# Performance work log

Measured on AMD Instinct MI355X. Metric: run time of the kernel, lower is better.

## Reference

```python
import jax, jax.numpy as jnp
import numpy as np

LAMBDA_0 = 1.0
EPS = 1e-6


def setup_inputs() -> dict:
    key = jax.random.key(0)
    ks = jax.random.split(key, 5)
    B, T, D, H = 4, 2048, 1024, 128
    x = jax.random.normal(ks[0], (B, T, D), dtype=jnp.float32)
    Wq = jax.random.normal(ks[1], (H, D), dtype=jnp.float32) * (D ** -0.5)
    Wk = jax.random.normal(ks[2], (H, D), dtype=jnp.float32) * (D ** -0.5)
    Wv = jax.random.normal(ks[3], (H, D), dtype=jnp.float32) * (D ** -0.5)
    Wo = jax.random.normal(ks[4], (D, H), dtype=jnp.float32) * (H ** -0.5)
    bq = jnp.zeros((H,), jnp.float32)
    bk = jnp.zeros((H,), jnp.float32)
    bv = jnp.zeros((H,), jnp.float32)
    bo = jnp.zeros((D,), jnp.float32)
    return {"x": x, "Wq": Wq, "bq": bq, "Wk": Wk, "bk": bk, "Wv": Wv, "bv": bv, "Wo": Wo, "bo": bo}


def reference(x, Wq, bq, Wk, bk, Wv, bv, Wo, bo):
    B, T, D = x.shape
    H = Wq.shape[0]
    # Projections for all timesteps at once (equivalent to per-step Linear calls)
    Q = jnp.einsum('btd,hd->bth', x, Wq) + bq
    K = jnp.einsum('btd,hd->bth', x, Wk) + bk
    V = jnp.einsum('btd,hd->bth', x, Wv) + bv

    A0 = jnp.broadcast_to(jnp.eye(H, dtype=jnp.float32) / LAMBDA_0, (B, H, H))  # (lambda_0 I)^-1
    M0 = jnp.zeros((B, H, H), jnp.float32)

    def step(carry, qkv):
        A, M = carry
        q, k, v = qkv                                  # each (B,H)
        s_t = jnp.sum(k * q, axis=-1, keepdims=True)   # (B,1)
        # PenaltyBuilder (rank-1): unit direction of k
        u = k / (jnp.linalg.norm(k, axis=-1, keepdims=True) + EPS)
        # Sherman-Morrison update: A <- A - (A u)(A u)^T / (1 + u^T A u)
        Au = jnp.einsum('bij,bj->bi', A, u)            # (B,H)
        denom = 1.0 + jnp.sum(u * Au, axis=-1, keepdims=True)  # (B,1)
        A = A - jnp.einsum('bi,bj->bij', Au, Au) / denom[..., None]
        # z = A_new @ u == Au / denom (exact identity, saves a matvec)
        z = Au / denom
        alpha = s_t * z                                # (B,H)
        M = M + jnp.einsum('bi,bj->bij', v, alpha)     # memory matrix accumulation
        o = jnp.einsum('bij,bj->bi', M, q)             # (B,H)
        return (A, M), o

    qkv = (jnp.swapaxes(Q, 0, 1), jnp.swapaxes(K, 0, 1), jnp.swapaxes(V, 0, 1))  # (T,B,H)
    _, O = jax.lax.scan(step, (A0, M0), qkv)
    O = jnp.swapaxes(O, 0, 1)                          # (B,T,H)
    return jnp.einsum('bth,dh->btd', O, Wo) + bo
```

## Files before the change

### kernel.cpp

```cpp
#include <hip/hip_runtime.h>
#include <math.h>

#define BB 4
#define TT 2048
#define DD 1024
#define HH 128
#define EPSF 1e-6f
#define BT (BB*TT)

__global__ __launch_bounds__(256) void proj_kernel(
    const float* __restrict__ x,
    const float* __restrict__ Wq, const float* __restrict__ bq,
    const float* __restrict__ Wk, const float* __restrict__ bk,
    const float* __restrict__ Wv, const float* __restrict__ bv,
    float* __restrict__ Q, float* __restrict__ K, float* __restrict__ V)
{
    const int which = blockIdx.y;
    const float* W    = (which == 0) ? Wq : (which == 1) ? Wk : Wv;
    const float* bias = (which == 0) ? bq : (which == 1) ? bk : bv;
    float* P          = (which == 0) ? Q  : (which == 1) ? K  : V;

    const int row0 = blockIdx.x * 64;

    __shared__ float xT[32][68];
    __shared__ float wT[32][132];

    const int tid = threadIdx.x;
    const int tx = tid & 15;
    const int ty = tid >> 4;

    float acc[4][8];
    #pragma unroll
    for (int i = 0; i < 4; i++)
        #pragma unroll
        for (int j = 0; j < 8; j++) acc[i][j] = 0.f;

    for (int k0 = 0; k0 < DD; k0 += 32) {
        #pragma unroll
        for (int l = 0; l < 2; l++) {
            int f = tid + l * 256;
            int r = f >> 3;
            int cg = f & 7;
            float4 v = *(const float4*)(x + (size_t)(row0 + r) * DD + k0 + cg * 4);
            xT[cg*4+0][r] = v.x; xT[cg*4+1][r] = v.y;
            xT[cg*4+2][r] = v.z; xT[cg*4+3][r] = v.w;
        }
        #pragma unroll
        for (int l = 0; l < 4; l++) {
            int f = tid + l * 256;
            int h = f >> 3;
            int cg = f & 7;
            float4 v = *(const float4*)(W + (size_t)h * DD + k0 + cg * 4);
            wT[cg*4+0][h] = v.x; wT[cg*4+1][h] = v.y;
            wT[cg*4+2][h] = v.z; wT[cg*4+3][h] = v.w;
        }
        __syncthreads();
        #pragma unroll
        for (int kk = 0; kk < 32; kk++) {
            float4 xv = *(const float4*)&xT[kk][ty * 4];
            float4 w0 = *(const float4*)&wT[kk][tx * 8];
            float4 w1 = *(const float4*)&wT[kk][tx * 8 + 4];
            float xa[4] = {xv.x, xv.y, xv.z, xv.w};
            float wa[8] = {w0.x, w0.y, w0.z, w0.w, w1.x, w1.y, w1.z, w1.w};
            #pragma unroll
            for (int i = 0; i < 4; i++)
                #pragma unroll
                for (int j = 0; j < 8; j++)
                    acc[i][j] += xa[i] * wa[j];
        }
        __syncthreads();
    }

    #pragma unroll
    for (int i = 0; i < 4; i++) {
        int row = row0 + ty * 4 + i;
        #pragma unroll
        for (int j = 0; j < 8; j++) acc[i][j] += bias[tx * 8 + j];
        float4 o0 = {acc[i][0], acc[i][1], acc[i][2], acc[i][3]};
        float4 o1 = {acc[i][4], acc[i][5], acc[i][6], acc[i][7]};
        *(float4*)(P + (size_t)row * HH + tx * 8)     = o0;
        *(float4*)(P + (size_t)row * HH + tx * 8 + 4) = o1;
    }
}

__global__ __launch_bounds__(512) void scan_kernel(
    const float* __restrict__ Q, const float* __restrict__ K,
    const float* __restrict__ V, float* __restrict__ O)
{
    const int b   = blockIdx.x;
    const int tid = threadIdx.x;
    const int r   = tid & 127;
    const int qd  = tid >> 7;
    const int c0  = qd * 32;
    const int lane = tid & 63;
    const int wave = tid >> 6;

    __shared__ float us[128], qs[128], vs[128], Aus[128];
    __shared__ float part[4][128];
    __shared__ float scal[2];

    float Areg[32], Mreg[32];
    #pragma unroll
    for (int j = 0; j < 32; j++) {
        Mreg[j] = 0.f;
        Areg[j] = (c0 + j == r) ? 1.0f : 0.0f;
    }

    const float* Qb = Q + (size_t)b * TT * HH;
    const float* Kb = K + (size_t)b * TT * HH;
    const float* Vb = V + (size_t)b * TT * HH;
    float*       Ob = O + (size_t)b * TT * HH;

    float s_reg = 0.f;

    for (int t = 0; t < TT; t++) {
        if (wave == 0) {
            float k0v = Kb[t * HH + lane];
            float k1v = Kb[t * HH + lane + 64];
            float q0v = Qb[t * HH + lane];
            float q1v = Qb[t * HH + lane + 64];
            float v0v = Vb[t * HH + lane];
            float v1v = Vb[t * HH + lane + 64];
            float pk2 = k0v * k0v + k1v * k1v;
            float pkq = k0v * q0v + k1v * q1v;
            #pragma unroll
            for (int off = 32; off; off >>= 1) {
                pk2 += __shfl_xor(pk2, off);
                pkq += __shfl_xor(pkq, off);
            }
            s_reg = pkq;
            float rn = 1.0f / (sqrtf(pk2) + EPSF);
            us[lane] = k0v * rn; us[lane + 64] = k1v * rn;
            qs[lane] = q0v;      qs[lane + 64] = q1v;
            vs[lane] = v0v;      vs[lane + 64] = v1v;
        }
        __syncthreads();

        {
            float p = 0.f;
            #pragma unroll
            for (int j = 0; j < 32; j += 4) {
                float4 uv = *(const float4*)&us[c0 + j];
                p += Areg[j]   * uv.x + Areg[j+1] * uv.y
                   + Areg[j+2] * uv.z + Areg[j+3] * uv.w;
            }
            part[qd][r] = p;
        }
        __syncthreads();

        if (wave == 0) {
            float au0 = part[0][lane] + part[1][lane] + part[2][lane] + part[3][lane];
            float au1 = part[0][lane+64] + part[1][lane+64] + part[2][lane+64] + part[3][lane+64];
            Aus[lane] = au0; Aus[lane + 64] = au1;
            float pd = us[lane] * au0 + us[lane + 64] * au1;
            #pragma unroll
            for (int off = 32; off; off >>= 1) pd += __shfl_xor(pd, off);
            float inv_d = 1.0f / (1.0f + pd);
            if (lane == 0) { scal[0] = inv_d; scal[1] = s_reg * inv_d; }
        }
        __syncthreads();

        {
            float inv_d = scal[0];
            float sa    = scal[1];
            float cA = Aus[r] * inv_d;
            float cM = vs[r] * sa;
            float op = 0.f;
            #pragma unroll
            for (int j = 0; j < 32; j += 4) {
                float4 av = *(const float4*)&Aus[c0 + j];
                float4 qv = *(const float4*)&qs[c0 + j];
                float aj[4] = {av.x, av.y, av.z, av.w};
                float qj[4] = {qv.x, qv.y, qv.z, qv.w};
                #pragma unroll
                for (int jj = 0; jj < 4; jj++) {
                    Areg[j + jj] -= cA * aj[jj];
                    Mreg[j + jj] += cM * aj[jj];
                    op += Mreg[j + jj] * qj[jj];
                }
            }
            part[qd][r] = op;
        }
        __syncthreads();

        if (wave == 0) {
            float o0 = part[0][lane] + part[1][lane] + part[2][lane] + part[3][lane];
            float o1 = part[0][lane+64] + part[1][lane+64] + part[2][lane+64] + part[3][lane+64];
            Ob[t * HH + lane]      = o0;
            Ob[t * HH + lane + 64] = o1;
        }
    }
}

__global__ __launch_bounds__(256) void out_kernel(
    const float* __restrict__ O, const float* __restrict__ Wo,
    const float* __restrict__ bo, float* __restrict__ out)
{
    const int row0 = blockIdx.x * 64;
    const int d0   = blockIdx.y * 128;

    __shared__ float oT[32][68];
    __shared__ float woT[32][132];

    const int tid = threadIdx.x;
    const int tx = tid & 15;
    const int ty = tid >> 4;

    float acc[4][8];
    #pragma unroll
    for (int i = 0; i < 4; i++)
        #pragma unroll
        for (int j = 0; j < 8; j++) acc[i][j] = 0.f;

    for (int k0 = 0; k0 < HH; k0 += 32) {
        #pragma unroll
        for (int l = 0; l < 2; l++) {
            int f = tid + l * 256;
            int r = f >> 3;
            int cg = f & 7;
            float4 v = *(const float4*)(O + (size_t)(row0 + r) * HH + k0 + cg * 4);
            oT[cg*4+0][r] = v.x; oT[cg*4+1][r] = v.y;
            oT[cg*4+2][r] = v.z; oT[cg*4+3][r] = v.w;
        }
        #pragma unroll
        for (int l = 0; l < 4; l++) {
            int f = tid + l * 256;
            int d = f >> 3;
            int cg = f & 7;
            float4 v = *(const float4*)(Wo + (size_t)(d0 + d) * HH + k0 + cg * 4);
            woT[cg*4+0][d] = v.x; woT[cg*4+1][d] = v.y;
            woT[cg*4+2][d] = v.z; woT[cg*4+3][d] = v.w;
        }
        __syncthreads();
        #pragma unroll
        for (int kk = 0; kk < 32; kk++) {
            float4 ov = *(const float4*)&oT[kk][ty * 4];
            float4 w0 = *(const float4*)&woT[kk][tx * 8];
            float4 w1 = *(const float4*)&woT[kk][tx * 8 + 4];
            float oa[4] = {ov.x, ov.y, ov.z, ov.w};
            float wa[8] = {w0.x, w0.y, w0.z, w0.w, w1.x, w1.y, w1.z, w1.w};
            #pragma unroll
            for (int i = 0; i < 4; i++)
                #pragma unroll
                for (int j = 0; j < 8; j++)
                    acc[i][j] += oa[i] * wa[j];
        }
        __syncthreads();
    }

    #pragma unroll
    for (int i = 0; i < 4; i++) {
        int row = row0 + ty * 4 + i;
        #pragma unroll
        for (int j = 0; j < 8; j++) acc[i][j] += bo[d0 + tx * 8 + j];
        float4 o0 = {acc[i][0], acc[i][1], acc[i][2], acc[i][3]};
        float4 o1 = {acc[i][4], acc[i][5], acc[i][6], acc[i][7]};
        *(float4*)(out + (size_t)row * DD + d0 + tx * 8)     = o0;
        *(float4*)(out + (size_t)row * DD + d0 + tx * 8 + 4) = o1;
    }
}

extern "C" void kernel_launch(void* const* d_in, const int* in_sizes, int n_in,
                              void* d_out, int out_size, void* d_ws, size_t ws_size,
                              hipStream_t stream) {
    const float* x  = (const float*)d_in[0];
    const float* Wq = (const float*)d_in[1];
    const float* bq = (const float*)d_in[2];
    const float* Wk = (const float*)d_in[3];
    const float* bk = (const float*)d_in[4];
    const float* Wv = (const float*)d_in[5];
    const float* bv = (const float*)d_in[6];
    const float* Wo = (const float*)d_in[7];
    const float* bo = (const float*)d_in[8];
    float* out = (float*)d_out;

    float* ws = (float*)d_ws;
    float* Q = ws;
    float* K = ws + (size_t)BT * HH;
    float* V = ws + (size_t)2 * BT * HH;
    float* O = ws + (size_t)3 * BT * HH;

    dim3 pgrid(BT / 64, 3);
    proj_kernel<<<pgrid, 256, 0, stream>>>(x, Wq, bq, Wk, bk, Wv, bv, Q, K, V);

    scan_kernel<<<BB, 512, 0, stream>>>(Q, K, V, O);

    dim3 ogrid(BT / 64, DD / 128);
    out_kernel<<<ogrid, 256, 0, stream>>>(O, Wo, bo, out);
}
```

Measured before the change: 3.963 ms.

## Remap scan threads to shuffle-reduce rows and cut barriers per step

The scan kernel's threads are remapped so the four threads sharing a matrix row sit in adjacent lanes. Their partial dot products can then be combined with warp shuffles instead of shared-memory partial arrays. The denominator is reduced per wave and combined through a small shared array. With double-buffered shared vectors this cuts the per-timestep barriers from four to two. The next step's K/Q/V loads are also prefetched into registers to hide global-load latency on the serial recurrence, at the cost of extra registers and slightly more complex indexing.

```diff
diff --git a/kernel.cpp b/kernel.cpp
--- a/kernel.cpp
+++ b/kernel.cpp
@@ -87,17 +87,17 @@
     const float* __restrict__ Q, const float* __restrict__ K,
     const float* __restrict__ V, float* __restrict__ O)
 {
-    const int b   = blockIdx.x;
-    const int tid = threadIdx.x;
-    const int r   = tid & 127;
-    const int qd  = tid >> 7;
-    const int c0  = qd * 32;
+    const int b    = blockIdx.x;
+    const int tid  = threadIdx.x;
+    const int r    = tid >> 2;
+    const int q4   = tid & 3;
+    const int c0   = q4 * 32;
     const int lane = tid & 63;
     const int wave = tid >> 6;
 
-    __shared__ float us[128], qs[128], vs[128], Aus[128];
-    __shared__ float part[4][128];
-    __shared__ float scal[2];
+    __shared__ float us[2][128], qs[2][128], vs[2][128], Aus[2][128];
+    __shared__ float dwave[2][8];
+    __shared__ float ss[2];
 
     float Areg[32], Mreg[32];
     #pragma unroll
@@ -111,16 +111,20 @@
     const float* Vb = V + (size_t)b * TT * HH;
     float*       Ob = O + (size_t)b * TT * HH;
 
-    float s_reg = 0.f;
+    float pk0 = 0.f, pk1 = 0.f, pq0 = 0.f, pq1 = 0.f, pv0 = 0.f, pv1 = 0.f;
+    if (wave == 0) {
+        pk0 = Kb[lane]; pk1 = Kb[lane + 64];
+        pq0 = Qb[lane]; pq1 = Qb[lane + 64];
+        pv0 = Vb[lane]; pv1 = Vb[lane + 64];
+    }
 
     for (int t = 0; t < TT; t++) {
+        const int buf = t & 1;
+
         if (wave == 0) {
-            float k0v = Kb[t * HH + lane];
-            float k1v = Kb[t * HH + lane + 64];
-            float q0v = Qb[t * HH + lane];
-            float q1v = Qb[t * HH + lane + 64];
-            float v0v = Vb[t * HH + lane];
-            float v1v = Vb[t * HH + lane + 64];
+            float k0v = pk0, k1v = pk1;
+            float q0v = pq0, q1v = pq1;
+            float v0v = pv0, v1v = pv1;
             float pk2 = k0v * k0v + k1v * k1v;
             float pkq = k0v * q0v + k1v * q1v;
             #pragma unroll
@@ -128,67 +132,64 @@
                 pk2 += __shfl_xor(pk2, off);
                 pkq += __shfl_xor(pkq, off);
             }
-            s_reg = pkq;
             float rn = 1.0f / (sqrtf(pk2) + EPSF);
-            us[lane] = k0v * rn; us[lane + 64] = k1v * rn;
-            qs[lane] = q0v;      qs[lane + 64] = q1v;
-            vs[lane] = v0v;      vs[lane + 64] = v1v;
-        }
-        __syncthreads();
-
-        {
-            float p = 0.f;
-            #pragma unroll
-            for (int j = 0; j < 32; j += 4) {
-                float4 uv = *(const float4*)&us[c0 + j];
-                p += Areg[j]   * uv.x + Areg[j+1] * uv.y
-                   + Areg[j+2] * uv.z + Areg[j+3] * uv.w;
+            us[buf][lane] = k0v * rn; us[buf][lane + 64] = k1v * rn;
+            qs[buf][lane] = q0v;      qs[buf][lane + 64] = q1v;
+            vs[buf][lane] = v0v;      vs[buf][lane + 64] = v1v;
+            if (lane == 0) ss[buf] = pkq;
+            if (t + 1 < TT) {
+                const int base = (t + 1) * HH + lane;
+                pk0 = Kb[base]; pk1 = Kb[base + 64];
+                pq0 = Qb[base]; pq1 = Qb[base + 64];
+                pv0 = Vb[base]; pv1 = Vb[base + 64];
             }
-            part[qd][r] = p;
-        }
-        __syncthreads();
-
-        if (wave == 0) {
-            float au0 = part[0][lane] + part[1][lane] + part[2][lane] + part[3][lane];
-            float au1 = part[0][lane+64] + part[1][lane+64] + part[2][lane+64] + part[3][lane+64];
-            Aus[lane] = au0; Aus[lane + 64] = au1;
-            float pd = us[lane] * au0 + us[lane + 64] * au1;
-            #pragma unroll
-            for (int off = 32; off; off >>= 1) pd += __shfl_xor(pd, off);
-            float inv_d = 1.0f / (1.0f + pd);
-            if (lane == 0) { scal[0] = inv_d; scal[1] = s_reg * inv_d; }
-        }
-        __syncthreads();
-
-        {
-            float inv_d = scal[0];
-            float sa    = scal[1];
-            float cA = Aus[r] * inv_d;
-            float cM = vs[r] * sa;
-            float op = 0.f;
-            #pragma unroll
-            for (int j = 0; j < 32; j += 4) {
-                float4 av = *(const float4*)&Aus[c0 + j];
-                float4 qv = *(const float4*)&qs[c0 + j];
-                float aj[4] = {av.x, av.y, av.z, av.w};
-                float qj[4] = {qv.x, qv.y, qv.z, qv.w};
-                #pragma unroll
-                for (int jj = 0; jj < 4; jj++) {
-                    Areg[j + jj] -= cA * aj[jj];
-                    Mreg[j + jj] += cM * aj[jj];
-                    op += Mreg[j + jj] * qj[jj];
-                }
-            }
-            part[qd][r] = op;
-        }
-        __syncthreads();
-
-        if (wave == 0) {
-            float o0 = part[0][lane] + part[1][lane] + part[2][lane] + part[3][lane];
-            float o1 = part[0][lane+64] + part[1][lane+64] + part[2][lane+64] + part[3][lane+64];
-            Ob[t * HH + lane]      = o0;
-            Ob[t * HH + lane + 64] = o1;
-        }
+        }
+        __syncthreads();
+
+        const float* ub = us[buf];
+        float p = 0.f;
+        #pragma unroll
+        for (int j = 0; j < 32; j += 4) {
+            float4 uv = *(const float4*)&ub[c0 + j];
+            p += Areg[j]   * uv.x + Areg[j+1] * uv.y
+               + Areg[j+2] * uv.z + Areg[j+3] * uv.w;
+        }
+        p += __shfl_xor(p, 1);
+        p += __shfl_xor(p, 2);
+        float dval = 0.f;
+        if (q4 == 0) {
+            Aus[buf][r] = p;
+            dval = ub[r] * p;
+        }
+        #pragma unroll
+        for (int off = 32; off; off >>= 1) dval += __shfl_xor(dval, off);
+        if (lane == 0) dwave[buf][wave] = dval;
+        __syncthreads();
+
+        float4 d0 = *(const float4*)&dwave[buf][0];
+        float4 d1 = *(const float4*)&dwave[buf][4];
+        float denom = 1.0f + d0.x + d0.y + d0.z + d0.w
+                           + d1.x + d1.y + d1.z + d1.w;
+        float inv_d = 1.0f / denom;
+        float sa    = ss[buf] * inv_d;
+
+        float cA = p * inv_d;
+        float cM = vs[buf][r] * sa;
+        const float* ab = Aus[buf];
+        const float* qb = qs[buf];
+        float o = 0.f;
+        #pragma unroll
+        for (int j = 0; j < 32; j += 4) {
+            float4 av = *(const float4*)&ab[c0 + j];
+            float4 qv = *(const float4*)&qb[c0 + j];
+            Areg[j]   -= cA * av.x;  Mreg[j]   += cM * av.x;  o += Mreg[j]   * qv.x;
+            Areg[j+1] -= cA * av.y;  Mreg[j+1] += cM * av.y;  o += Mreg[j+1] * qv.y;
+            Areg[j+2] -= cA * av.z;  Mreg[j+2] += cM * av.z;  o += Mreg[j+2] * qv.z;
+            Areg[j+3] -= cA * av.w;  Mreg[j+3] += cM * av.w;  o += Mreg[j+3] * qv.w;
+        }
+        o += __shfl_xor(o, 1);
+        o += __shfl_xor(o, 2);
+        if (q4 == 0) Ob[t * HH + r] = o;
     }
 }
 
```

Measured after the change: 3.479 ms. 1.14x faster.

## Replace sequential rank-1 scan with chunked blocked Sherman-Morrison and parallel memory accumulation

Applied to the files above, without the earlier changes.

The per-timestep scan is replaced by a chunked algorithm. A pass over chunks of 64 steps computes the alpha vectors with a blocked form of the rank-1 inverse updates: a Gram matrix, an in-LDS LDL-style elimination, then one rank-64 update of A per chunk. The linear memory recurrence is then split into two parallel kernels, per-chunk outer-product sums and prefix-combined outputs using a causal intra-chunk matrix. This swaps thousands of barrier-bound tiny steps for matrix-shaped work, at the cost of a different floating-point summation order and aliasing the output buffer and K as scratch.

```diff
diff --git a/kernel.cpp b/kernel.cpp
--- a/kernel.cpp
+++ b/kernel.cpp
@@ -7,6 +7,10 @@
 #define HH 128
 #define EPSF 1e-6f
 #define BT (BB*TT)
+#define CH 64
+#define NCH (TT/CH)
+#define CP 128
+#define NCP (TT/CP)
 
 __global__ __launch_bounds__(256) void proj_kernel(
     const float* __restrict__ x,
@@ -83,111 +87,344 @@
     }
 }
 
-__global__ __launch_bounds__(512) void scan_kernel(
+__global__ __launch_bounds__(256) void pass1_kernel(
     const float* __restrict__ Q, const float* __restrict__ K,
-    const float* __restrict__ V, float* __restrict__ O)
+    float* __restrict__ alpha)
 {
-    const int b   = blockIdx.x;
+    extern __shared__ float lds[];
+    float* A0 = lds;
+    float* Us = A0 + 128*132;
+    float* Ws = Us + 64*132;
+    float* Fs = Ws + 64*132;
+    float* ss = Fs + 64*68;
+    float* ls = ss + 64;
+
+    const int b = blockIdx.x;
     const int tid = threadIdx.x;
-    const int r   = tid & 127;
-    const int qd  = tid >> 7;
-    const int c0  = qd * 32;
-    const int lane = tid & 63;
-    const int wave = tid >> 6;
-
-    __shared__ float us[128], qs[128], vs[128], Aus[128];
-    __shared__ float part[4][128];
-    __shared__ float scal[2];
-
-    float Areg[32], Mreg[32];
-    #pragma unroll
-    for (int j = 0; j < 32; j++) {
-        Mreg[j] = 0.f;
-        Areg[j] = (c0 + j == r) ? 1.0f : 0.0f;
-    }
-
     const float* Qb = Q + (size_t)b * TT * HH;
     const float* Kb = K + (size_t)b * TT * HH;
-    const float* Vb = V + (size_t)b * TT * HH;
-    float*       Ob = O + (size_t)b * TT * HH;
-
-    float s_reg = 0.f;
-
-    for (int t = 0; t < TT; t++) {
-        if (wave == 0) {
-            float k0v = Kb[t * HH + lane];
-            float k1v = Kb[t * HH + lane + 64];
-            float q0v = Qb[t * HH + lane];
-            float q1v = Qb[t * HH + lane + 64];
-            float v0v = Vb[t * HH + lane];
-            float v1v = Vb[t * HH + lane + 64];
-            float pk2 = k0v * k0v + k1v * k1v;
-            float pkq = k0v * q0v + k1v * q1v;
-            #pragma unroll
-            for (int off = 32; off; off >>= 1) {
-                pk2 += __shfl_xor(pk2, off);
-                pkq += __shfl_xor(pkq, off);
-            }
-            s_reg = pkq;
-            float rn = 1.0f / (sqrtf(pk2) + EPSF);
-            us[lane] = k0v * rn; us[lane + 64] = k1v * rn;
-            qs[lane] = q0v;      qs[lane + 64] = q1v;
-            vs[lane] = v0v;      vs[lane + 64] = v1v;
-        }
-        __syncthreads();
+    float* ab = alpha + (size_t)b * TT * HH;
+
+    for (int idx = tid; idx < 128*132; idx += 256) A0[idx] = 0.f;
+    __syncthreads();
+    for (int r = tid; r < 128; r += 256) A0[r*132 + r] = 1.0f;
+    __syncthreads();
+
+    const int tx = tid & 15;
+    const int ty = tid >> 4;
+
+    for (int ch = 0; ch < NCH; ch++) {
+        const int t0 = ch * CH;
 
         {
-            float p = 0.f;
-            #pragma unroll
-            for (int j = 0; j < 32; j += 4) {
-                float4 uv = *(const float4*)&us[c0 + j];
-                p += Areg[j]   * uv.x + Areg[j+1] * uv.y
-                   + Areg[j+2] * uv.z + Areg[j+3] * uv.w;
-            }
-            part[qd][r] = p;
-        }
-        __syncthreads();
-
-        if (wave == 0) {
-            float au0 = part[0][lane] + part[1][lane] + part[2][lane] + part[3][lane];
-            float au1 = part[0][lane+64] + part[1][lane+64] + part[2][lane+64] + part[3][lane+64];
-            Aus[lane] = au0; Aus[lane + 64] = au1;
-            float pd = us[lane] * au0 + us[lane + 64] * au1;
-            #pragma unroll
-            for (int off = 32; off; off >>= 1) pd += __shfl_xor(pd, off);
-            float inv_d = 1.0f / (1.0f + pd);
-            if (lane == 0) { scal[0] = inv_d; scal[1] = s_reg * inv_d; }
+            const int i = tid >> 2, p = tid & 3, cp = p * 32;
+            const float* krow = Kb + (size_t)(t0 + i) * HH + cp;
+            const float* qrow = Qb + (size_t)(t0 + i) * HH + cp;
+            float4 kv[8];
+            float kk = 0.f, kq = 0.f;
+            #pragma unroll
+            for (int j = 0; j < 8; j++) {
+                kv[j] = *(const float4*)(krow + 4*j);
+                float4 qv = *(const float4*)(qrow + 4*j);
+                kk += kv[j].x*kv[j].x + kv[j].y*kv[j].y + kv[j].z*kv[j].z + kv[j].w*kv[j].w;
+                kq += kv[j].x*qv.x + kv[j].y*qv.y + kv[j].z*qv.z + kv[j].w*qv.w;
+            }
+            kk += __shfl_xor(kk, 1); kk += __shfl_xor(kk, 2);
+            kq += __shfl_xor(kq, 1); kq += __shfl_xor(kq, 2);
+            float rn = 1.0f / (sqrtf(kk) + EPSF);
+            #pragma unroll
+            for (int j = 0; j < 8; j++) {
+                float4 u = {kv[j].x*rn, kv[j].y*rn, kv[j].z*rn, kv[j].w*rn};
+                *(float4*)&Us[i*132 + cp + 4*j] = u;
+            }
+            if (p == 0) ss[i] = kq;
         }
         __syncthreads();
 
         {
-            float inv_d = scal[0];
-            float sa    = scal[1];
-            float cA = Aus[r] * inv_d;
-            float cM = vs[r] * sa;
-            float op = 0.f;
-            #pragma unroll
-            for (int j = 0; j < 32; j += 4) {
-                float4 av = *(const float4*)&Aus[c0 + j];
-                float4 qv = *(const float4*)&qs[c0 + j];
-                float aj[4] = {av.x, av.y, av.z, av.w};
-                float qj[4] = {qv.x, qv.y, qv.z, qv.w};
-                #pragma unroll
-                for (int jj = 0; jj < 4; jj++) {
-                    Areg[j + jj] -= cA * aj[jj];
-                    Mreg[j + jj] += cM * aj[jj];
-                    op += Mreg[j + jj] * qj[jj];
+            const int c0 = tx * 8;
+            float acc[4][8];
+            #pragma unroll
+            for (int r = 0; r < 4; r++)
+                #pragma unroll
+                for (int j = 0; j < 8; j++) acc[r][j] = 0.f;
+            for (int k0 = 0; k0 < HH; k0 += 4) {
+                float4 uu[4];
+                #pragma unroll
+                for (int r = 0; r < 4; r++)
+                    uu[r] = *(const float4*)&Us[(ty + 16*r)*132 + k0];
+                #pragma unroll
+                for (int kk = 0; kk < 4; kk++) {
+                    float4 a0 = *(const float4*)&A0[(k0+kk)*132 + c0];
+                    float4 a1 = *(const float4*)&A0[(k0+kk)*132 + c0 + 4];
+                    float av[8] = {a0.x,a0.y,a0.z,a0.w,a1.x,a1.y,a1.z,a1.w};
+                    #pragma unroll
+                    for (int r = 0; r < 4; r++) {
+                        float u = (kk==0)?uu[r].x:(kk==1)?uu[r].y:(kk==2)?uu[r].z:uu[r].w;
+                        #pragma unroll
+                        for (int jx = 0; jx < 8; jx++) acc[r][jx] += u * av[jx];
+                    }
                 }
             }
-            part[qd][r] = op;
-        }
-        __syncthreads();
-
-        if (wave == 0) {
-            float o0 = part[0][lane] + part[1][lane] + part[2][lane] + part[3][lane];
-            float o1 = part[0][lane+64] + part[1][lane+64] + part[2][lane+64] + part[3][lane+64];
-            Ob[t * HH + lane]      = o0;
-            Ob[t * HH + lane + 64] = o1;
+            #pragma unroll
+            for (int r = 0; r < 4; r++) {
+                int row = ty + 16*r;
+                *(float4*)&Ws[row*132 + c0]     = make_float4(acc[r][0],acc[r][1],acc[r][2],acc[r][3]);
+                *(float4*)&Ws[row*132 + c0 + 4] = make_float4(acc[r][4],acc[r][5],acc[r][6],acc[r][7]);
+            }
+        }
+        __syncthreads();
+
+        {
+            float acc2[4][4];
+            #pragma unroll
+            for (int r = 0; r < 4; r++)
+                #pragma unroll
+                for (int s = 0; s < 4; s++) acc2[r][s] = 0.f;
+            for (int k0 = 0; k0 < HH; k0 += 4) {
+                float4 wv[4], uv[4];
+                #pragma unroll
+                for (int r = 0; r < 4; r++) wv[r] = *(const float4*)&Ws[(ty+16*r)*132 + k0];
+                #pragma unroll
+                for (int s = 0; s < 4; s++) uv[s] = *(const float4*)&Us[(tx+16*s)*132 + k0];
+                #pragma unroll
+                for (int r = 0; r < 4; r++)
+                    #pragma unroll
+                    for (int s = 0; s < 4; s++)
+                        acc2[r][s] += wv[r].x*uv[s].x + wv[r].y*uv[s].y
+                                    + wv[r].z*uv[s].z + wv[r].w*uv[s].w;
+            }
+            #pragma unroll
+            for (int r = 0; r < 4; r++)
+                #pragma unroll
+                for (int s = 0; s < 4; s++) {
+                    int i = ty + 16*r, j = tx + 16*s;
+                    Fs[i*68 + j] = acc2[r][s] + ((i == j) ? 1.0f : 0.0f);
+                }
+        }
+        __syncthreads();
+
+        for (int j = 0; j < CH; j++) {
+            float dinv = 1.0f / Fs[j*68 + j];
+            if (tid > j && tid < CH) ls[tid] = Fs[tid*68 + j] * dinv;
+            __syncthreads();
+            const int cg = tid & 7;
+            const int ri = tid >> 3;
+            const int cbase = cg * 24;
+            #pragma unroll
+            for (int pass = 0; pass < 2; pass++) {
+                int i = j + 1 + ri + pass*32;
+                if (i < CH) {
+                    float l = ls[i];
+                    #pragma unroll
+                    for (int cc = 0; cc < 24; cc += 4) {
+                        int c = cbase + cc;
+                        if (c < 64) {
+                            float4 rj = *(const float4*)&Fs[j*68 + c];
+                            float4 rv = *(float4*)&Fs[i*68 + c];
+                            rv.x -= l*rj.x; rv.y -= l*rj.y; rv.z -= l*rj.z; rv.w -= l*rj.w;
+                            *(float4*)&Fs[i*68 + c] = rv;
+                        } else {
+                            float4 rj = *(const float4*)&Ws[j*132 + (c-64)];
+                            float4 rv = *(float4*)&Ws[i*132 + (c-64)];
+                            rv.x -= l*rj.x; rv.y -= l*rj.y; rv.z -= l*rj.z; rv.w -= l*rj.w;
+                            *(float4*)&Ws[i*132 + (c-64)] = rv;
+                        }
+                    }
+                }
+            }
+            __syncthreads();
+        }
+
+        {
+            const int i = tid >> 2, p = tid & 3, cp = p * 32;
+            float d = Fs[i*68 + i];
+            float dinv = 1.0f / d;
+            float ca = ss[i] * dinv;
+            float cs = sqrtf(dinv);
+            float* wrow = &Ws[i*132 + cp];
+            float* arow = ab + (size_t)(t0 + i) * HH + cp;
+            #pragma unroll
+            for (int jj = 0; jj < 32; jj += 4) {
+                float4 w = *(const float4*)&wrow[jj];
+                *(float4*)&arow[jj] = make_float4(ca*w.x, ca*w.y, ca*w.z, ca*w.w);
+                *(float4*)&wrow[jj] = make_float4(cs*w.x, cs*w.y, cs*w.z, cs*w.w);
+            }
+        }
+        __syncthreads();
+
+        if (ch != NCH - 1) {
+            const int r0 = (tid >> 4) * 8, c0 = (tid & 15) * 8;
+            float acc[8][8];
+            #pragma unroll
+            for (int a = 0; a < 8; a++)
+                #pragma unroll
+                for (int bb = 0; bb < 8; bb++) acc[a][bb] = 0.f;
+            for (int i = 0; i < CH; i++) {
+                float4 ra = *(const float4*)&Ws[i*132 + r0];
+                float4 rb = *(const float4*)&Ws[i*132 + r0 + 4];
+                float4 ca_ = *(const float4*)&Ws[i*132 + c0];
+                float4 cb = *(const float4*)&Ws[i*132 + c0 + 4];
+                float rr[8] = {ra.x,ra.y,ra.z,ra.w,rb.x,rb.y,rb.z,rb.w};
+                float cc[8] = {ca_.x,ca_.y,ca_.z,ca_.w,cb.x,cb.y,cb.z,cb.w};
+                #pragma unroll
+                for (int a = 0; a < 8; a++)
+                    #pragma unroll
+                    for (int bb = 0; bb < 8; bb++) acc[a][bb] += rr[a]*cc[bb];
+            }
+            #pragma unroll
+            for (int a = 0; a < 8; a++) {
+                #pragma unroll
+                for (int b4 = 0; b4 < 8; b4 += 4) {
+                    float4 v = *(float4*)&A0[(r0+a)*132 + c0 + b4];
+                    v.x -= acc[a][b4+0]; v.y -= acc[a][b4+1];
+                    v.z -= acc[a][b4+2]; v.w -= acc[a][b4+3];
+                    *(float4*)&A0[(r0+a)*132 + c0 + b4] = v;
+                }
+            }
+        }
+        __syncthreads();
+    }
+}
+
+__global__ __launch_bounds__(256) void chunk_sum_kernel(
+    const float* __restrict__ alpha, const float* __restrict__ V,
+    float* __restrict__ S)
+{
+    const int bidx = blockIdx.x;
+    const int b = bidx >> 4, c = bidx & 15;
+    const int tid = threadIdx.x;
+    const int x0 = (tid >> 4) * 8, h0 = (tid & 15) * 8;
+    const float* arow = alpha + ((size_t)b * TT + c * CP) * HH;
+    const float* vrow = V + ((size_t)b * TT + c * CP) * HH;
+    float acc[8][8];
+    #pragma unroll
+    for (int a = 0; a < 8; a++)
+        #pragma unroll
+        for (int h = 0; h < 8; h++) acc[a][h] = 0.f;
+    for (int t = 0; t < CP; t++) {
+        float4 a0 = *(const float4*)&arow[(size_t)t*HH + x0];
+        float4 a1 = *(const float4*)&arow[(size_t)t*HH + x0 + 4];
+        float4 v0 = *(const float4*)&vrow[(size_t)t*HH + h0];
+        float4 v1 = *(const float4*)&vrow[(size_t)t*HH + h0 + 4];
+        float aa[8] = {a0.x,a0.y,a0.z,a0.w,a1.x,a1.y,a1.z,a1.w};
+        float vv[8] = {v0.x,v0.y,v0.z,v0.w,v1.x,v1.y,v1.z,v1.w};
+        #pragma unroll
+        for (int a = 0; a < 8; a++)
+            #pragma unroll
+            for (int h = 0; h < 8; h++) acc[a][h] += aa[a]*vv[h];
+    }
+    float* Sblk = S + (size_t)(b * NCP + c) * HH * HH;
+    #pragma unroll
+    for (int a = 0; a < 8; a++) {
+        #pragma unroll
+        for (int h4 = 0; h4 < 8; h4 += 4)
+            *(float4*)&Sblk[(size_t)(x0+a)*HH + h0 + h4] =
+                make_float4(acc[a][h4],acc[a][h4+1],acc[a][h4+2],acc[a][h4+3]);
+    }
+}
+
+__global__ __launch_bounds__(256) void chunk_out_kernel(
+    const float* __restrict__ Qm, const float* __restrict__ alpha,
+    const float* __restrict__ V, const float* __restrict__ S,
+    float* __restrict__ O)
+{
+    extern __shared__ float lds[];
+    float* Mt = lds;
+    float* Pt = Mt + 128*132;
+
+    const int bidx = blockIdx.x;
+    const int b = bidx >> 4, c = bidx & 15;
+    const int tid = threadIdx.x;
+    const float* qrow = Qm + ((size_t)b * TT + c * CP) * HH;
+    const float* arow = alpha + ((size_t)b * TT + c * CP) * HH;
+    const float* vrow = V + ((size_t)b * TT + c * CP) * HH;
+
+    for (int idx4 = tid; idx4 < (HH*HH)/4; idx4 += 256) {
+        int x = idx4 >> 5;
+        int h4 = (idx4 & 31) * 4;
+        float4 s = make_float4(0.f,0.f,0.f,0.f);
+        for (int cp = 0; cp < c; cp++) {
+            float4 v = *(const float4*)&S[(size_t)(b*NCP+cp)*HH*HH + (size_t)x*HH + h4];
+            s.x += v.x; s.y += v.y; s.z += v.z; s.w += v.w;
+        }
+        *(float4*)&Mt[x*132 + h4] = s;
+    }
+
+    {
+        const int s0 = (tid >> 4) * 8, t0l = (tid & 15) * 8;
+        float accB[8][8];
+        #pragma unroll
+        for (int a = 0; a < 8; a++)
+            #pragma unroll
+            for (int t = 0; t < 8; t++) accB[a][t] = 0.f;
+        for (int k0 = 0; k0 < HH; k0 += 4) {
+            float4 qv[8], av[8];
+            #pragma unroll
+            for (int t = 0; t < 8; t++) qv[t] = *(const float4*)&qrow[(size_t)(t0l+t)*HH + k0];
+            #pragma unroll
+            for (int a = 0; a < 8; a++) av[a] = *(const float4*)&arow[(size_t)(s0+a)*HH + k0];
+            #pragma unroll
+            for (int a = 0; a < 8; a++)
+                #pragma unroll
+                for (int t = 0; t < 8; t++)
+                    accB[a][t] += av[a].x*qv[t].x + av[a].y*qv[t].y
+                                + av[a].z*qv[t].z + av[a].w*qv[t].w;
+        }
+        __syncthreads();
+        #pragma unroll
+        for (int a = 0; a < 8; a++)
+            #pragma unroll
+            for (int t = 0; t < 8; t++) {
+                int sg = s0 + a, tg = t0l + t;
+                Pt[sg*132 + tg] = (sg <= tg) ? accB[a][t] : 0.f;
+            }
+    }
+    __syncthreads();
+
+    {
+        const int tr0 = (tid >> 4) * 8, h0 = (tid & 15) * 8;
+        float acc[8][8];
+        #pragma unroll
+        for (int a = 0; a < 8; a++)
+            #pragma unroll
+            for (int h = 0; h < 8; h++) acc[a][h] = 0.f;
+        for (int s = 0; s < CP; s++) {
+            float4 p0 = *(const float4*)&Pt[s*132 + tr0];
+            float4 p1 = *(const float4*)&Pt[s*132 + tr0 + 4];
+            float4 v0 = *(const float4*)&vrow[(size_t)s*HH + h0];
+            float4 v1 = *(const float4*)&vrow[(size_t)s*HH + h0 + 4];
+            float pp[8] = {p0.x,p0.y,p0.z,p0.w,p1.x,p1.y,p1.z,p1.w};
+            float vv[8] = {v0.x,v0.y,v0.z,v0.w,v1.x,v1.y,v1.z,v1.w};
+            #pragma unroll
+            for (int a = 0; a < 8; a++)
+                #pragma unroll
+                for (int h = 0; h < 8; h++) acc[a][h] += pp[a]*vv[h];
+        }
+        for (int x0 = 0; x0 < HH; x0 += 4) {
+            float4 qv[8];
+            #pragma unroll
+            for (int a = 0; a < 8; a++) qv[a] = *(const float4*)&qrow[(size_t)(tr0+a)*HH + x0];
+            #pragma unroll
+            for (int kk = 0; kk < 4; kk++) {
+                float4 m0 = *(const float4*)&Mt[(x0+kk)*132 + h0];
+                float4 m1 = *(const float4*)&Mt[(x0+kk)*132 + h0 + 4];
+                float mm[8] = {m0.x,m0.y,m0.z,m0.w,m1.x,m1.y,m1.z,m1.w};
+                #pragma unroll
+                for (int a = 0; a < 8; a++) {
+                    float qq = (kk==0)?qv[a].x:(kk==1)?qv[a].y:(kk==2)?qv[a].z:qv[a].w;
+                    #pragma unroll
+                    for (int h = 0; h < 8; h++) acc[a][h] += qq*mm[h];
+                }
+            }
+        }
+        float* orow = O + ((size_t)b * TT + c * CP) * HH;
+        #pragma unroll
+        for (int a = 0; a < 8; a++) {
+            #pragma unroll
+            for (int h4 = 0; h4 < 8; h4 += 4)
+                *(float4*)&orow[(size_t)(tr0+a)*HH + h0 + h4] =
+                    make_float4(acc[a][h4],acc[a][h4+1],acc[a][h4+2],acc[a][h4+3]);
         }
     }
 }
@@ -278,12 +515,20 @@
     float* Q = ws;
     float* K = ws + (size_t)BT * HH;
     float* V = ws + (size_t)2 * BT * HH;
-    float* O = ws + (size_t)3 * BT * HH;
+    float* S = ws + (size_t)3 * BT * HH;
+    float* O = K;
+    float* alpha = out;
 
     dim3 pgrid(BT / 64, 3);
     proj_kernel<<<pgrid, 256, 0, stream>>>(x, Wq, bq, Wk, bk, Wv, bv, Q, K, V);
 
-    scan_kernel<<<BB, 512, 0, stream>>>(Q, K, V, O);
+    const size_t p1_lds = (size_t)(128*132 + 64*132 + 64*132 + 64*68 + 64 + 64) * 4;
+    pass1_kernel<<<BB, 256, p1_lds, stream>>>(Q, K, alpha);
+
+    chunk_sum_kernel<<<BB * NCP, 256, 0, stream>>>(alpha, V, S);
+
+    const size_t k4_lds = (size_t)(2 * 128 * 132) * 4;
+    chunk_out_kernel<<<BB * NCP, 256, k4_lds, stream>>>(Q, alpha, V, S, O);
 
     dim3 ogrid(BT / 64, DD / 128);
     out_kernel<<<ogrid, 256, 0, stream>>>(O, Wo, bo, out);
```

Result: slower. 4.808 ms (+21.3%).
